# Performance work log

Hardware: AMD Instinct MI355X
Metric: run time of the kernel (lower is better)

The kernel has to match this reference:

```python
import jax, jax.numpy as jnp
import numpy as np

A, B, D, L = 256, 64, 768, 2  # annotators, batch, hidden, num_labels
G1, G2 = 4, 8                 # groups per attribute


def setup_inputs() -> dict:
    key = jax.random.key(0)
    ks = jax.random.split(key, 9)
    s = 1.0 / np.sqrt(D)
    return {
        "pooled": jax.random.normal(ks[0], (B, D), jnp.float32),
        "W1": jax.random.normal(ks[1], (G1, D, D), jnp.float32) * s,
        "b1": jax.random.normal(ks[2], (G1, D), jnp.float32) * s,
        "W2": jax.random.normal(ks[3], (G2, D, D), jnp.float32) * s,
        "b2": jax.random.normal(ks[4], (G2, D), jnp.float32) * s,
        "Wh": jax.random.normal(ks[5], (A, D, L), jnp.float32) * s,
        "bh": jax.random.normal(ks[6], (A, L), jnp.float32) * s,
        "g1_idx": jax.random.randint(ks[7], (A,), 0, G1),
        "g2_idx": jax.random.randint(ks[8], (A,), 0, G2),
    }


def reference(pooled, W1, b1, W2, b2, Wh, bh, g1_idx, g2_idx):
    # Attribute 1: every annotator with the same group shares the transform,
    # so compute once per group then gather (avoids A redundant GEMMs).
    h_g = jnp.einsum('bd,gde->gbe', pooled, W1) + b1[:, None, :]   # [G1, B, D]
    h = h_g[g1_idx]                                                # [A, B, D]
    # Attribute 2: input now differs per annotator -> grouped GEMM via gathered weights.
    h = jnp.einsum('abd,ade->abe', h, W2[g2_idx]) + b2[g2_idx][:, None, :]  # [A, B, D]
    # Per-annotator classification heads.
    logits = jnp.einsum('abd,adl->abl', h, Wh) + bh[:, None, :]    # [A, B, L]
    # Match torch layout: logits[batch, annotator, label]
    return jnp.transpose(logits, (1, 0, 2))                        # [B, A, L]
```

## Files before the change

kernel.cpp:

```cpp
#include <hip/hip_runtime.h>
#include <hip/hip_bf16.h>

#define AN 256
#define BN 64
#define DN 768
#define LN 2
#define G1N 4
#define G2N 8
#define KI (DN / 32)

typedef __attribute__((ext_vector_type(8))) short short8;
typedef __attribute__((ext_vector_type(4))) short bf16x4;
typedef __attribute__((ext_vector_type(4))) float floatx4;

static __device__ __forceinline__ unsigned short f2bf(float f) {
    union { float f; unsigned int u; } v; v.f = f;
    unsigned int r = v.u + 0x7FFF + ((v.u >> 16) & 1);
    return (unsigned short)(r >> 16);
}

__global__ __launch_bounds__(256) void k_prep(
    const float* __restrict__ pooled, const float* __restrict__ W1,
    const float* __restrict__ b2, const float* __restrict__ Wh,
    const float* __restrict__ bh,
    const int* __restrict__ g1i, const int* __restrict__ g2i,
    unsigned short* __restrict__ W1t, unsigned short* __restrict__ Whp,
    unsigned short* __restrict__ pooled_bf, float* __restrict__ bc,
    int* __restrict__ n1, int* __restrict__ n2,
    int* __restrict__ lst1, int* __restrict__ sidx2)
{
    const int tid = threadIdx.x, bx = blockIdx.x;

    if (bx < 576) {
        const int g = bx / 144, t = bx % 144;
        const int d0 = (t / 12) * 64, e0 = (t % 12) * 64;
        const float* src = W1 + (size_t)g * DN * DN;
        __shared__ float tile[64][65];
        const int r = tid >> 4, c = (tid & 15) * 4;
        #pragma unroll
        for (int i = 0; i < 4; ++i) {
            float4 v = *(const float4*)(src + (size_t)(d0 + r + 16 * i) * DN + e0 + c);
            tile[r + 16 * i][c + 0] = v.x; tile[r + 16 * i][c + 1] = v.y;
            tile[r + 16 * i][c + 2] = v.z; tile[r + 16 * i][c + 3] = v.w;
        }
        __syncthreads();
        #pragma unroll
        for (int i = 0; i < 4; ++i) {
            bf16x4 v;
            #pragma unroll
            for (int j = 0; j < 4; ++j) v[j] = (short)f2bf(tile[c + j][r + 16 * i]);
            *(bf16x4*)(W1t + ((size_t)g * DN + e0 + r + 16 * i) * DN + d0 + c) = v;
        }
        return;
    }

    if (bx < 584) {
        const int i0 = (bx - 576) * 6144;
        for (int i = i0 + tid; i < i0 + 6144; i += 256)
            pooled_bf[i] = f2bf(pooled[i]);

        const int aa = tid >> 3, j = tid & 7;
        const int a = (bx - 576) * 32 + aa;
        const int gv2 = g2i[a];
        const float* whp = Wh + (size_t)a * (DN * LN);
        const float* b2p = b2 + gv2 * DN;
        float acc0 = 0.f, acc1 = 0.f;
        #pragma unroll 4
        for (int i = 0; i < 48; ++i) {
            int e = j * 96 + i * 2;
            float4 w4 = *(const float4*)(whp + e * 2);
            float2 bv = *(const float2*)(b2p + e);
            acc0 += bv.x * w4.x + bv.y * w4.z;
            acc1 += bv.x * w4.y + bv.y * w4.w;
        }
        #pragma unroll
        for (int off = 4; off; off >>= 1) {
            acc0 += __shfl_down(acc0, off, 64);
            acc1 += __shfl_down(acc1, off, 64);
        }
        if (j == 0) {
            bc[a * 2 + 0] = acc0 + bh[a * 2 + 0];
            bc[a * 2 + 1] = acc1 + bh[a * 2 + 1];
        }
        return;
    }

    if (bx == 584) {
        __shared__ int g1s[AN], g2s[AN];
        __shared__ int c1s[G1N], c2s[G2N];
        g1s[tid] = g1i[tid];
        g2s[tid] = g2i[tid];
        if (tid < G1N) c1s[tid] = 0;
        if (tid < G2N) c2s[tid] = 0;
        __syncthreads();
        int s = 0, my2 = g2s[tid];
        for (int a2 = 0; a2 < tid; ++a2) s += (g2s[a2] == my2);
        sidx2[tid] = s;
        atomicAdd(&c2s[my2], 1);
        int p1 = atomicAdd(&c1s[g1s[tid]], 1);
        lst1[g1s[tid] * 256 + p1] = tid;
        __syncthreads();
        if (tid < G1N) n1[tid] = c1s[tid];
        if (tid < G2N) n2[tid] = c2s[tid];
        return;
    }

    {
        const int a = bx - 585;
        __shared__ int g2s[AN];
        g2s[tid] = g2i[tid];
        __syncthreads();
        int s = 0, my2 = g2s[a];
        for (int a2 = 0; a2 < a; ++a2) s += (g2s[a2] == my2);
        const size_t rp = ((size_t)my2 * 128 + s) * 2;
        const float* wa = Wh + (size_t)a * (DN * LN);
        #pragma unroll
        for (int i = 0; i < 3; ++i) {
            int e = i * 256 + tid;
            float2 v = *(const float2*)(wa + e * 2);
            Whp[rp * DN + e]       = f2bf(v.x);
            Whp[(rp + 1) * DN + e] = f2bf(v.y);
        }
    }
}

__global__ __launch_bounds__(256) void k_mid(
    const float* __restrict__ W2, const float* __restrict__ b1,
    const unsigned short* __restrict__ W1t,
    const unsigned short* __restrict__ Whp,
    const unsigned short* __restrict__ pooled_bf,
    const int* __restrict__ n2,
    unsigned short* __restrict__ h1, unsigned short* __restrict__ Wcs)
{
    const int tid  = threadIdx.x;
    const int lane = tid & 63, wave = tid >> 6;
    const int nn   = lane & 15, quad = lane >> 4;

    if (blockIdx.y < G1N) {
        const int g = blockIdx.y, e0 = blockIdx.x * 64;
        const int e = e0 + wave * 16 + nn;
        const unsigned short* Bt = W1t + ((size_t)g * DN + e) * DN + quad * 8;
        const unsigned short* Ap = pooled_bf + (size_t)nn * DN + quad * 8;
        floatx4 acc[4] = {{0,0,0,0},{0,0,0,0},{0,0,0,0},{0,0,0,0}};
        #pragma unroll
        for (int kk = 0; kk < KI; ++kk) {
            short8 bf = *(const short8*)(Bt + kk * 32);
            #pragma unroll
            for (int mt = 0; mt < 4; ++mt) {
                short8 af = *(const short8*)(Ap + (size_t)(mt * 16) * DN + kk * 32);
                acc[mt] = __builtin_amdgcn_mfma_f32_16x16x32_bf16(af, bf, acc[mt], 0, 0, 0);
            }
        }
        const float bv = b1[g * DN + e];
        #pragma unroll
        for (int mt = 0; mt < 4; ++mt)
            #pragma unroll
            for (int r = 0; r < 4; ++r)
                h1[(size_t)g * BN * DN + (size_t)(mt * 16 + quad * 4 + r) * DN + e] =
                    f2bf(acc[mt][r] + bv);
    } else {
        const int g = blockIdx.y - G1N;
        const int mbase = blockIdx.x * 64;
        const int cols = 2 * n2[g];
        const int m_row = mbase + wave * 16 + nn;

        const float* ap = W2 + ((size_t)g * DN + m_row) * DN + quad * 8;
        short8 Areg[KI];
        #pragma unroll
        for (int kk = 0; kk < KI; ++kk) {
            float4 a0 = *(const float4*)(ap + kk * 32);
            float4 a1 = *(const float4*)(ap + kk * 32 + 4);
            short8 af;
            af[0] = (short)f2bf(a0.x); af[1] = (short)f2bf(a0.y);
            af[2] = (short)f2bf(a0.z); af[3] = (short)f2bf(a0.w);
            af[4] = (short)f2bf(a1.x); af[5] = (short)f2bf(a1.y);
            af[6] = (short)f2bf(a1.z); af[7] = (short)f2bf(a1.w);
            Areg[kk] = af;
        }

        const unsigned short* Bbase = Whp + (size_t)(g * 256) * DN;
        for (int c0 = 0; c0 < cols; c0 += 16) {
            const unsigned short* Brow = Bbase + (size_t)(c0 + nn) * DN + quad * 8;
            floatx4 acc = {0, 0, 0, 0};
            #pragma unroll
            for (int kk = 0; kk < KI; ++kk) {
                short8 bf = *(const short8*)(Brow + kk * 32);
                acc = __builtin_amdgcn_mfma_f32_16x16x32_bf16(Areg[kk], bf, acc, 0, 0, 0);
            }
            const int c = c0 + nn;
            if (c < cols) {
                const int dbase = mbase + wave * 16 + quad * 4;
                bf16x4 v;
                #pragma unroll
                for (int r = 0; r < 4; ++r) v[r] = (short)f2bf(acc[r]);
                *(bf16x4*)(Wcs + (size_t)(g * 256 + c) * DN + dbase) = v;
            }
        }
    }
}

__global__ __launch_bounds__(256) void k_last(
    const unsigned short* __restrict__ h1, const unsigned short* __restrict__ Wcs,
    const float* __restrict__ bc, const int* __restrict__ n1,
    const int* __restrict__ lst1, const int* __restrict__ sidx2,
    const int* __restrict__ g2i, float* __restrict__ out)
{
    const int g = blockIdx.y;
    const int cols = 2 * n1[g];
    const int nt0 = blockIdx.x * 16;
    if (nt0 >= cols) return;

    const int tid = threadIdx.x;
    const int lane = tid & 63, wave = tid >> 6;
    const int nn = lane & 15, quad = lane >> 4;

    const int c = nt0 + nn;
    const bool valid = (c < cols);
    const int cl = valid ? c : (cols - 1);
    const int a = lst1[g * 256 + (cl >> 1)];
    const int l = cl & 1;
    const int rp = (g2i[a] * 128 + sidx2[a]) * 2 + l;

    const unsigned short* hg = h1 + (size_t)g * BN * DN + (size_t)(wave * 16 + nn) * DN + quad * 8;
    const unsigned short* wp = Wcs + (size_t)rp * DN + quad * 8;

    floatx4 acc = {0, 0, 0, 0};
    #pragma unroll
    for (int kk = 0; kk < KI; ++kk) {
        short8 af = *(const short8*)(hg + kk * 32);
        short8 bf = *(const short8*)(wp + kk * 32);
        acc = __builtin_amdgcn_mfma_f32_16x16x32_bf16(af, bf, acc, 0, 0, 0);
    }
    if (valid) {
        const float bv = bc[a * 2 + l];
        #pragma unroll
        for (int r = 0; r < 4; ++r)
            out[(size_t)(wave * 16 + quad * 4 + r) * (AN * LN) + a * 2 + l] = acc[r] + bv;
    }
}

extern "C" void kernel_launch(void* const* d_in, const int* in_sizes, int n_in,
                              void* d_out, int out_size, void* d_ws, size_t ws_size,
                              hipStream_t stream) {
    const float* pooled = (const float*)d_in[0];
    const float* W1     = (const float*)d_in[1];
    const float* b1     = (const float*)d_in[2];
    const float* W2     = (const float*)d_in[3];
    const float* b2     = (const float*)d_in[4];
    const float* Wh     = (const float*)d_in[5];
    const float* bh     = (const float*)d_in[6];
    const int*   g1i    = (const int*)d_in[7];
    const int*   g2i    = (const int*)d_in[8];
    float* out = (float*)d_out;

    char* ws = (char*)d_ws;
    float* bc   = (float*)ws;             ws += 512 * 4;
    int*   n1   = (int*)ws;               ws += 4 * 4;
    int*   n2   = (int*)ws;               ws += 8 * 4;
    int*   lst1 = (int*)ws;               ws += 4 * 256 * 4;
    int*   sidx2= (int*)ws;               ws += 256 * 4;
    unsigned short* pooled_bf = (unsigned short*)ws;  ws += (size_t)BN * DN * 2;
    unsigned short* h1        = (unsigned short*)ws;  ws += (size_t)G1N * BN * DN * 2;
    unsigned short* W1t       = (unsigned short*)ws;  ws += (size_t)G1N * DN * DN * 2;
    unsigned short* Whp       = (unsigned short*)ws;  ws += (size_t)G2N * 256 * DN * 2;
    unsigned short* Wcs       = (unsigned short*)ws;

    dim3 blk(256);
    k_prep<<<dim3(841),    blk, 0, stream>>>(pooled, W1, b2, Wh, bh, g1i, g2i,
                                             W1t, Whp, pooled_bf, bc, n1, n2, lst1, sidx2);
    k_mid <<<dim3(12, 12), blk, 0, stream>>>(W2, b1, W1t, Whp, pooled_bf, n2, h1, Wcs);
    k_last<<<dim3(32, 4),  blk, 0, stream>>>(h1, Wcs, bc, n1, lst1, sidx2, g2i, out);
}
```

Before: 135.6 us.

## Fuse three kernels into one cooperative persistent kernel with grid syncs

Replaces the separate prep, mid and last kernel launches with a single cooperative kernel of 256 blocks. The blocks loop over the 841 prep jobs, then run the mid and last stages separated by grid-wide barriers. This removes two kernel launches and the inter-kernel gaps. The cost is lower parallelism in the prep stage, idle blocks during the later stages, and grid-sync overhead. The separate shared-memory arrays of each stage now coexist in one kernel, which raises the LDS footprint per block.

New measurement: 223.7 us. +65.0%, slower.

```diff
diff --git a/kernel.cpp b/kernel.cpp
--- a/kernel.cpp
+++ b/kernel.cpp
@@ -1,5 +1,7 @@
 #include <hip/hip_runtime.h>
-#include <hip/hip_bf16.h>
+#include <hip/hip_cooperative_groups.h>
+
+namespace cg = cooperative_groups;
 
 #define AN 256
 #define BN 64
@@ -19,22 +21,36 @@
     return (unsigned short)(r >> 16);
 }
 
-__global__ __launch_bounds__(256) void k_prep(
-    const float* __restrict__ pooled, const float* __restrict__ W1,
-    const float* __restrict__ b2, const float* __restrict__ Wh,
-    const float* __restrict__ bh,
-    const int* __restrict__ g1i, const int* __restrict__ g2i,
-    unsigned short* __restrict__ W1t, unsigned short* __restrict__ Whp,
-    unsigned short* __restrict__ pooled_bf, float* __restrict__ bc,
-    int* __restrict__ n1, int* __restrict__ n2,
-    int* __restrict__ lst1, int* __restrict__ sidx2)
-{
-    const int tid = threadIdx.x, bx = blockIdx.x;
+struct Params {
+    const float* __restrict__ pooled;
+    const float* __restrict__ W1;
+    const float* __restrict__ b1;
+    const float* __restrict__ W2;
+    const float* __restrict__ b2;
+    const float* __restrict__ Wh;
+    const float* __restrict__ bh;
+    const int*   __restrict__ g1i;
+    const int*   __restrict__ g2i;
+    float*       __restrict__ out;
+    unsigned short* __restrict__ W1t;
+    unsigned short* __restrict__ Whp;
+    unsigned short* __restrict__ pooled_bf;
+    float* __restrict__ bc;
+    int*   __restrict__ n1;
+    int*   __restrict__ n2;
+    int*   __restrict__ lst1;
+    int*   __restrict__ sidx2;
+    unsigned short* __restrict__ h1;
+    unsigned short* __restrict__ Wcs;
+};
+
+static __device__ __forceinline__ void prep_job(int bx, const Params& p) {
+    const int tid = threadIdx.x;
 
     if (bx < 576) {
         const int g = bx / 144, t = bx % 144;
         const int d0 = (t / 12) * 64, e0 = (t % 12) * 64;
-        const float* src = W1 + (size_t)g * DN * DN;
+        const float* src = p.W1 + (size_t)g * DN * DN;
         __shared__ float tile[64][65];
         const int r = tid >> 4, c = (tid & 15) * 4;
         #pragma unroll
@@ -49,7 +65,7 @@
             bf16x4 v;
             #pragma unroll
             for (int j = 0; j < 4; ++j) v[j] = (short)f2bf(tile[c + j][r + 16 * i]);
-            *(bf16x4*)(W1t + ((size_t)g * DN + e0 + r + 16 * i) * DN + d0 + c) = v;
+            *(bf16x4*)(p.W1t + ((size_t)g * DN + e0 + r + 16 * i) * DN + d0 + c) = v;
         }
         return;
     }
@@ -57,13 +73,13 @@
     if (bx < 584) {
         const int i0 = (bx - 576) * 6144;
         for (int i = i0 + tid; i < i0 + 6144; i += 256)
-            pooled_bf[i] = f2bf(pooled[i]);
+            p.pooled_bf[i] = f2bf(p.pooled[i]);
 
         const int aa = tid >> 3, j = tid & 7;
         const int a = (bx - 576) * 32 + aa;
-        const int gv2 = g2i[a];
-        const float* whp = Wh + (size_t)a * (DN * LN);
-        const float* b2p = b2 + gv2 * DN;
+        const int gv2 = p.g2i[a];
+        const float* whp = p.Wh + (size_t)a * (DN * LN);
+        const float* b2p = p.b2 + gv2 * DN;
         float acc0 = 0.f, acc1 = 0.f;
         #pragma unroll 4
         for (int i = 0; i < 48; ++i) {
@@ -79,8 +95,8 @@
             acc1 += __shfl_down(acc1, off, 64);
         }
         if (j == 0) {
-            bc[a * 2 + 0] = acc0 + bh[a * 2 + 0];
-            bc[a * 2 + 1] = acc1 + bh[a * 2 + 1];
+            p.bc[a * 2 + 0] = acc0 + p.bh[a * 2 + 0];
+            p.bc[a * 2 + 1] = acc1 + p.bh[a * 2 + 1];
         }
         return;
     }
@@ -88,59 +104,52 @@
     if (bx == 584) {
         __shared__ int g1s[AN], g2s[AN];
         __shared__ int c1s[G1N], c2s[G2N];
-        g1s[tid] = g1i[tid];
-        g2s[tid] = g2i[tid];
+        g1s[tid] = p.g1i[tid];
+        g2s[tid] = p.g2i[tid];
         if (tid < G1N) c1s[tid] = 0;
         if (tid < G2N) c2s[tid] = 0;
         __syncthreads();
         int s = 0, my2 = g2s[tid];
         for (int a2 = 0; a2 < tid; ++a2) s += (g2s[a2] == my2);
-        sidx2[tid] = s;
+        p.sidx2[tid] = s;
         atomicAdd(&c2s[my2], 1);
         int p1 = atomicAdd(&c1s[g1s[tid]], 1);
-        lst1[g1s[tid] * 256 + p1] = tid;
-        __syncthreads();
-        if (tid < G1N) n1[tid] = c1s[tid];
-        if (tid < G2N) n2[tid] = c2s[tid];
+        p.lst1[g1s[tid] * 256 + p1] = tid;
+        __syncthreads();
+        if (tid < G1N) p.n1[tid] = c1s[tid];
+        if (tid < G2N) p.n2[tid] = c2s[tid];
         return;
     }
 
     {
         const int a = bx - 585;
         __shared__ int g2s[AN];
-        g2s[tid] = g2i[tid];
+        g2s[tid] = p.g2i[tid];
         __syncthreads();
         int s = 0, my2 = g2s[a];
         for (int a2 = 0; a2 < a; ++a2) s += (g2s[a2] == my2);
         const size_t rp = ((size_t)my2 * 128 + s) * 2;
-        const float* wa = Wh + (size_t)a * (DN * LN);
+        const float* wa = p.Wh + (size_t)a * (DN * LN);
         #pragma unroll
         for (int i = 0; i < 3; ++i) {
             int e = i * 256 + tid;
             float2 v = *(const float2*)(wa + e * 2);
-            Whp[rp * DN + e]       = f2bf(v.x);
-            Whp[(rp + 1) * DN + e] = f2bf(v.y);
-        }
-    }
-}
-
-__global__ __launch_bounds__(256) void k_mid(
-    const float* __restrict__ W2, const float* __restrict__ b1,
-    const unsigned short* __restrict__ W1t,
-    const unsigned short* __restrict__ Whp,
-    const unsigned short* __restrict__ pooled_bf,
-    const int* __restrict__ n2,
-    unsigned short* __restrict__ h1, unsigned short* __restrict__ Wcs)
-{
+            p.Whp[rp * DN + e]       = f2bf(v.x);
+            p.Whp[(rp + 1) * DN + e] = f2bf(v.y);
+        }
+    }
+}
+
+static __device__ __forceinline__ void mid_job(int bx, int by, const Params& p) {
     const int tid  = threadIdx.x;
     const int lane = tid & 63, wave = tid >> 6;
     const int nn   = lane & 15, quad = lane >> 4;
 
-    if (blockIdx.y < G1N) {
-        const int g = blockIdx.y, e0 = blockIdx.x * 64;
+    if (by < G1N) {
+        const int g = by, e0 = bx * 64;
         const int e = e0 + wave * 16 + nn;
-        const unsigned short* Bt = W1t + ((size_t)g * DN + e) * DN + quad * 8;
-        const unsigned short* Ap = pooled_bf + (size_t)nn * DN + quad * 8;
+        const unsigned short* Bt = p.W1t + ((size_t)g * DN + e) * DN + quad * 8;
+        const unsigned short* Ap = p.pooled_bf + (size_t)nn * DN + quad * 8;
         floatx4 acc[4] = {{0,0,0,0},{0,0,0,0},{0,0,0,0},{0,0,0,0}};
         #pragma unroll
         for (int kk = 0; kk < KI; ++kk) {
@@ -151,20 +160,20 @@
                 acc[mt] = __builtin_amdgcn_mfma_f32_16x16x32_bf16(af, bf, acc[mt], 0, 0, 0);
             }
         }
-        const float bv = b1[g * DN + e];
+        const float bv = p.b1[g * DN + e];
         #pragma unroll
         for (int mt = 0; mt < 4; ++mt)
             #pragma unroll
             for (int r = 0; r < 4; ++r)
-                h1[(size_t)g * BN * DN + (size_t)(mt * 16 + quad * 4 + r) * DN + e] =
+                p.h1[(size_t)g * BN * DN + (size_t)(mt * 16 + quad * 4 + r) * DN + e] =
                     f2bf(acc[mt][r] + bv);
     } else {
-        const int g = blockIdx.y - G1N;
-        const int mbase = blockIdx.x * 64;
-        const int cols = 2 * n2[g];
+        const int g = by - G1N;
+        const int mbase = bx * 64;
+        const int cols = 2 * p.n2[g];
         const int m_row = mbase + wave * 16 + nn;
 
-        const float* ap = W2 + ((size_t)g * DN + m_row) * DN + quad * 8;
+        const float* ap = p.W2 + ((size_t)g * DN + m_row) * DN + quad * 8;
         short8 Areg[KI];
         #pragma unroll
         for (int kk = 0; kk < KI; ++kk) {
@@ -178,7 +187,7 @@
             Areg[kk] = af;
         }
 
-        const unsigned short* Bbase = Whp + (size_t)(g * 256) * DN;
+        const unsigned short* Bbase = p.Whp + (size_t)(g * 256) * DN;
         for (int c0 = 0; c0 < cols; c0 += 16) {
             const unsigned short* Brow = Bbase + (size_t)(c0 + nn) * DN + quad * 8;
             floatx4 acc = {0, 0, 0, 0};
@@ -193,21 +202,16 @@
                 bf16x4 v;
                 #pragma unroll
                 for (int r = 0; r < 4; ++r) v[r] = (short)f2bf(acc[r]);
-                *(bf16x4*)(Wcs + (size_t)(g * 256 + c) * DN + dbase) = v;
+                *(bf16x4*)(p.Wcs + (size_t)(g * 256 + c) * DN + dbase) = v;
             }
         }
     }
 }
 
-__global__ __launch_bounds__(256) void k_last(
-    const unsigned short* __restrict__ h1, const unsigned short* __restrict__ Wcs,
-    const float* __restrict__ bc, const int* __restrict__ n1,
-    const int* __restrict__ lst1, const int* __restrict__ sidx2,
-    const int* __restrict__ g2i, float* __restrict__ out)
-{
-    const int g = blockIdx.y;
-    const int cols = 2 * n1[g];
-    const int nt0 = blockIdx.x * 16;
+static __device__ __forceinline__ void last_job(int bx, int by, const Params& p) {
+    const int g = by;
+    const int cols = 2 * p.n1[g];
+    const int nt0 = bx * 16;
     if (nt0 >= cols) return;
 
     const int tid = threadIdx.x;
@@ -217,12 +221,12 @@
     const int c = nt0 + nn;
     const bool valid = (c < cols);
     const int cl = valid ? c : (cols - 1);
-    const int a = lst1[g * 256 + (cl >> 1)];
+    const int a = p.lst1[g * 256 + (cl >> 1)];
     const int l = cl & 1;
-    const int rp = (g2i[a] * 128 + sidx2[a]) * 2 + l;
-
-    const unsigned short* hg = h1 + (size_t)g * BN * DN + (size_t)(wave * 16 + nn) * DN + quad * 8;
-    const unsigned short* wp = Wcs + (size_t)rp * DN + quad * 8;
+    const int rp = (p.g2i[a] * 128 + p.sidx2[a]) * 2 + l;
+
+    const unsigned short* hg = p.h1 + (size_t)g * BN * DN + (size_t)(wave * 16 + nn) * DN + quad * 8;
+    const unsigned short* wp = p.Wcs + (size_t)rp * DN + quad * 8;
 
     floatx4 acc = {0, 0, 0, 0};
     #pragma unroll
@@ -232,42 +236,58 @@
         acc = __builtin_amdgcn_mfma_f32_16x16x32_bf16(af, bf, acc, 0, 0, 0);
     }
     if (valid) {
-        const float bv = bc[a * 2 + l];
+        const float bv = p.bc[a * 2 + l];
         #pragma unroll
         for (int r = 0; r < 4; ++r)
-            out[(size_t)(wave * 16 + quad * 4 + r) * (AN * LN) + a * 2 + l] = acc[r] + bv;
-    }
+            p.out[(size_t)(wave * 16 + quad * 4 + r) * (AN * LN) + a * 2 + l] = acc[r] + bv;
+    }
+}
+
+__global__ __launch_bounds__(256) void fused(Params p) {
+    cg::grid_group grid = cg::this_grid();
+
+    for (int job = blockIdx.x; job < 841; job += 256) {
+        prep_job(job, p);
+        __syncthreads();
+    }
+
+    grid.sync();
+
+    if (blockIdx.x < 144) mid_job(blockIdx.x % 12, blockIdx.x / 12, p);
+
+    grid.sync();
+
+    if (blockIdx.x < 128) last_job(blockIdx.x & 31, blockIdx.x >> 5, p);
 }
 
 extern "C" void kernel_launch(void* const* d_in, const int* in_sizes, int n_in,
                               void* d_out, int out_size, void* d_ws, size_t ws_size,
                               hipStream_t stream) {
-    const float* pooled = (const float*)d_in[0];
-    const float* W1     = (const float*)d_in[1];
-    const float* b1     = (const float*)d_in[2];
-    const float* W2     = (const float*)d_in[3];
-    const float* b2     = (const float*)d_in[4];
-    const float* Wh     = (const float*)d_in[5];
-    const float* bh     = (const float*)d_in[6];
-    const int*   g1i    = (const int*)d_in[7];
-    const int*   g2i    = (const int*)d_in[8];
-    float* out = (float*)d_out;
+    Params p;
+    p.pooled = (const float*)d_in[0];
+    p.W1     = (const float*)d_in[1];
+    p.b1     = (const float*)d_in[2];
+    p.W2     = (const float*)d_in[3];
+    p.b2     = (const float*)d_in[4];
+    p.Wh     = (const float*)d_in[5];
+    p.bh     = (const float*)d_in[6];
+    p.g1i    = (const int*)d_in[7];
+    p.g2i    = (const int*)d_in[8];
+    p.out    = (float*)d_out;
 
     char* ws = (char*)d_ws;
-    float* bc   = (float*)ws;             ws += 512 * 4;
-    int*   n1   = (int*)ws;               ws += 4 * 4;
-    int*   n2   = (int*)ws;               ws += 8 * 4;
-    int*   lst1 = (int*)ws;               ws += 4 * 256 * 4;
-    int*   sidx2= (int*)ws;               ws += 256 * 4;
-    unsigned short* pooled_bf = (unsigned short*)ws;  ws += (size_t)BN * DN * 2;
-    unsigned short* h1        = (unsigned short*)ws;  ws += (size_t)G1N * BN * DN * 2;
-    unsigned short* W1t       = (unsigned short*)ws;  ws += (size_t)G1N * DN * DN * 2;
-    unsigned short* Whp       = (unsigned short*)ws;  ws += (size_t)G2N * 256 * DN * 2;
-    unsigned short* Wcs       = (unsigned short*)ws;
-
-    dim3 blk(256);
-    k_prep<<<dim3(841),    blk, 0, stream>>>(pooled, W1, b2, Wh, bh, g1i, g2i,
-                                             W1t, Whp, pooled_bf, bc, n1, n2, lst1, sidx2);
-    k_mid <<<dim3(12, 12), blk, 0, stream>>>(W2, b1, W1t, Whp, pooled_bf, n2, h1, Wcs);
-    k_last<<<dim3(32, 4),  blk, 0, stream>>>(h1, Wcs, bc, n1, lst1, sidx2, g2i, out);
-}
+    p.bc    = (float*)ws;             ws += 512 * 4;
+    p.n1    = (int*)ws;               ws += 4 * 4;
+    p.n2    = (int*)ws;               ws += 8 * 4;
+    p.lst1  = (int*)ws;               ws += 4 * 256 * 4;
+    p.sidx2 = (int*)ws;               ws += 256 * 4;
+    p.pooled_bf = (unsigned short*)ws;  ws += (size_t)BN * DN * 2;
+    p.h1        = (unsigned short*)ws;  ws += (size_t)G1N * BN * DN * 2;
+    p.W1t       = (unsigned short*)ws;  ws += (size_t)G1N * DN * DN * 2;
+    p.Whp       = (unsigned short*)ws;  ws += (size_t)G2N * 256 * DN * 2;
+    p.Wcs       = (unsigned short*)ws;
+
+    void* args[] = { (void*)&p };
+    (void)hipLaunchCooperativeKernel((const void*)fused, dim3(256), dim3(256),
+                                     args, 0, stream);
+}
```
